# Kernel optimization log

Hardware: AMD Instinct MI355X
Metric: run time of the kernel (lower is better)

The kernel has to match this reference:

```python
import jax, jax.numpy as jnp
import numpy as np

E = 128  # embed_size


def setup_inputs() -> dict:
    key = jax.random.key(0)
    ks = jax.random.split(key, 20)
    NU, NI, NEV = 100000, 50000, 4096
    s = 0.05  # weight scale so softplus(dot) stays well-conditioned
    inp = {
        "user_emb": jax.random.normal(ks[0], (NU, E), jnp.float32) * s,
        "item_emb": jax.random.normal(ks[1], (NI, E), jnp.float32) * s,
        "ugru_wi": jax.random.normal(ks[2], (3 * E, E), jnp.float32) * s,
        "ugru_wh": jax.random.normal(ks[3], (3 * E, E), jnp.float32) * s,
        "ugru_bi": jax.random.normal(ks[4], (3 * E,), jnp.float32) * s,
        "ugru_bh": jax.random.normal(ks[5], (3 * E,), jnp.float32) * s,
        "igru_wi": jax.random.normal(ks[6], (3 * E, E), jnp.float32) * s,
        "igru_wh": jax.random.normal(ks[7], (3 * E, E), jnp.float32) * s,
        "igru_bi": jax.random.normal(ks[8], (3 * E,), jnp.float32) * s,
        "igru_bh": jax.random.normal(ks[9], (3 * E,), jnp.float32) * s,
        "t1_w": jax.random.normal(ks[10], (E, 2 * E), jnp.float32) * s,
        "t1_b": jax.random.normal(ks[11], (E,), jnp.float32) * s,
        "t2_w": jax.random.normal(ks[12], (32, E), jnp.float32) * s,
        "t2_b": jax.random.normal(ks[13], (32,), jnp.float32) * s,
        "t3_w": jax.random.normal(ks[14], (1, 32), jnp.float32) * s,
        "t3_b": jax.random.normal(ks[15], (1,), jnp.float32) * s,
        "user_ids": jax.random.randint(ks[16], (NEV,), 0, NU, jnp.int32),
        "item_ids": jax.random.randint(ks[17], (NEV,), 0, NI, jnp.int32),
    }
    return inp


def _gru(x, h, wi, wh, bi, bh):
    # torch.nn.GRUCell math, single sample: x,h [E]; wi,wh [3E,E]
    gi = wi @ x + bi
    gh = wh @ h + bh
    ir, iz, inn = jnp.split(gi, 3)
    hr, hz, hn = jnp.split(gh, 3)
    r = jax.nn.sigmoid(ir + hr)
    z = jax.nn.sigmoid(iz + hz)
    n = jnp.tanh(inn + r * hn)
    return (1.0 - z) * n + z * h


def reference(user_emb, item_emb, ugru_wi, ugru_wh, ugru_bi, ugru_bh,
              igru_wi, igru_wh, igru_bi, igru_bh,
              t1_w, t1_b, t2_w, t2_b, t3_w, t3_b,
              user_ids, item_ids):
    # Sequential event processing: per-event gather of user/item embedding,
    # Rayleigh base compatibility score, MLP (transForm1/2/3) branch score,
    # coupled GRUCell updates scattered back into the embedding tables.
    def step(carry, ev):
        U, V = carry
        u_id, i_id = ev
        u = U[u_id]          # [E] gather (dict-cache lookup in original)
        v = V[i_id]          # [E]
        comp = jax.nn.softplus(jnp.dot(u, v)) + 1e-10  # base_compatibility
        loss = -jnp.log(comp)                           # -log p(event)
        cat = jnp.concatenate([u, v])                   # [2E]
        h = jax.nn.relu(t1_w @ cat + t1_b)              # transForm1 + act
        h = jax.nn.relu(t2_w @ h + t2_b)                # transForm2 + act
        score = jax.nn.sigmoid(t3_w @ h + t3_b)[0]      # transForm3
        nu = _gru(v, u, ugru_wi, ugru_wh, ugru_bi, ugru_bh)  # user_cell
        nv = _gru(u, v, igru_wi, igru_wh, igru_bi, igru_bh)  # item_cell
        U = U.at[u_id].set(nu)  # coevolution scatter
        V = V.at[i_id].set(nv)
        return (U, V), jnp.stack([loss, score])

    (_, _), outs = jax.lax.scan(step, (user_emb, item_emb),
                                (user_ids, item_ids))
    return outs  # [num_events, 2] : (-log comp, branch score)
```

## Files before the change

kernel.cpp:

```cpp
#include <hip/hip_runtime.h>
#include <math.h>

#define EMB 128
#define MAXEV 4096
#define GEV 16

struct Hdr { int nl0; int nl1; int ncomp2; };

typedef __attribute__((ext_vector_type(8))) short bf16x8;
typedef __attribute__((ext_vector_type(4))) float f32x4;

__device__ __forceinline__ float sigmoidf_(float x) { return 1.0f / (1.0f + expf(-x)); }
__device__ __forceinline__ float softplusf_(float x) {
    return (x > 0.f) ? x + log1pf(expf(-x)) : log1pf(expf(x));
}
__device__ __forceinline__ unsigned short f2bf(float f) {
    unsigned int u = __float_as_uint(f);
    u += 0x7FFFu + ((u >> 16) & 1u);
    return (unsigned short)(u >> 16);
}
__device__ __forceinline__ float bf2f(unsigned short s) {
    return __uint_as_float((unsigned int)s << 16);
}

__global__ __launch_bounds__(64) void prev_kernel(
    const int* __restrict__ uids, const int* __restrict__ iids,
    int* __restrict__ prevu, int* __restrict__ previ, int nev,
    const float* __restrict__ Wuh, const float* __restrict__ Wii,
    const float* __restrict__ Wui, const float* __restrict__ Wih,
    const float* __restrict__ T1w, const float* __restrict__ T2w,
    unsigned short* __restrict__ wb_uh, unsigned short* __restrict__ wb_ii,
    unsigned short* __restrict__ wb_ui, unsigned short* __restrict__ wb_ih,
    unsigned short* __restrict__ t1wb, unsigned short* __restrict__ t2wb)
{
    int t = blockIdx.x;
    int lane = threadIdx.x;

    {
        int gid = t * 64 + lane;
        if (gid < 58368) {
            const float* src; unsigned short* dst; int q;
            if (gid < 49152) {
                int m = gid / 12288; q = gid - m * 12288;
                src = (m == 0) ? Wuh : (m == 1) ? Wii : (m == 2) ? Wui : Wih;
                dst = (m == 0) ? wb_uh : (m == 1) ? wb_ii : (m == 2) ? wb_ui : wb_ih;
            } else if (gid < 57344) { q = gid - 49152; src = T1w; dst = t1wb; }
            else                    { q = gid - 57344; src = T2w; dst = t2wb; }
            float4 v = ((const float4*)src)[q];
            *(ushort4*)(dst + (size_t)q * 4) =
                make_ushort4(f2bf(v.x), f2bf(v.y), f2bf(v.z), f2bf(v.w));
        }
    }

    if (t >= nev) return;
    int myu = uids[t], myi = iids[t];
    int bu = -1, bi = -1;
    for (int j = lane; j < t; j += 64) {
        if (uids[j] == myu) bu = j;
        if (iids[j] == myi) bi = j;
    }
    for (int off = 32; off; off >>= 1) {
        bu = max(bu, __shfl_xor(bu, off));
        bi = max(bi, __shfl_xor(bi, off));
    }
    if (lane == 0) { prevu[t] = bu; previ[t] = bi; }
}

__global__ __launch_bounds__(1024) void setup_kernel(
    const int* __restrict__ prevu, const int* __restrict__ previ,
    int* __restrict__ order0, int* __restrict__ order1,
    int* __restrict__ tail2Order, int* __restrict__ compStart,
    Hdr* __restrict__ hdr, int nev)
{
    __shared__ int   lab[MAXEV];
    __shared__ int   tmpT[MAXEV];
    __shared__ int   t2l[MAXEV];
    __shared__ short slev[MAXEV];
    __shared__ int   schanged, sn0, sn1, sn2, sntl;

    int tid = threadIdx.x;
    for (int t = tid; t < nev; t += 1024) slev[t] = 0;
    if (tid == 0) { sn0 = 0; sn1 = 0; sn2 = 0; sntl = 0; }
    __syncthreads();

    for (int t = tid; t < nev; t += 1024) {
        if (prevu[t] >= 0 || previ[t] >= 0) tmpT[atomicAdd(&sntl, 1)] = t;
        else                                 order0[atomicAdd(&sn0, 1)] = t;
    }
    __syncthreads();
    int ntl = sntl;

    for (int it = 0; it < nev; ++it) {
        if (tid == 0) schanged = 0;
        __syncthreads();
        for (int i = tid; i < ntl; i += 1024) {
            int t = tmpT[i];
            int pu = prevu[t], pi = previ[t];
            int nl = 0;
            if (pu >= 0) nl = slev[pu] + 1;
            if (pi >= 0) { int c = slev[pi] + 1; nl = nl > c ? nl : c; }
            if (nl > (int)slev[t]) { slev[t] = (short)nl; schanged = 1; }
        }
        __syncthreads();
        if (!schanged) break;
        __syncthreads();
    }

    for (int i = tid; i < ntl; i += 1024) {
        int t = tmpT[i];
        if (slev[t] == 1)      order1[atomicAdd(&sn1, 1)] = t;
        else if (slev[t] >= 2) t2l[atomicAdd(&sn2, 1)] = t;
    }
    __syncthreads();
    int n2 = sn2;

    for (int i = tid; i < n2; i += 1024) lab[t2l[i]] = t2l[i];
    __syncthreads();
    for (int it = 0; it < nev; ++it) {
        if (tid == 0) schanged = 0;
        __syncthreads();
        for (int i = tid; i < n2; i += 1024) {
            int t = t2l[i];
            int m = lab[t];
            int pu = prevu[t], pi = previ[t];
            bool eu = (pu >= 0 && slev[pu] >= 2);
            bool ei = (pi >= 0 && slev[pi] >= 2);
            if (eu) m = min(m, lab[pu]);
            if (ei) m = min(m, lab[pi]);
            if (m < lab[t]) { atomicMin(&lab[t], m); schanged = 1; }
            if (eu && m < lab[pu]) { atomicMin(&lab[pu], m); schanged = 1; }
            if (ei && m < lab[pi]) { atomicMin(&lab[pi], m); schanged = 1; }
        }
        __syncthreads();
        if (!schanged) break;
        __syncthreads();
    }

    for (int i = tid; i < n2; i += 1024) tmpT[i] = (lab[t2l[i]] << 12) | t2l[i];
    __syncthreads();
    for (int i = tid; i < n2; i += 1024) {
        int k = tmpT[i], r = 0;
        for (int j = 0; j < n2; ++j) r += (tmpT[j] < k);
        tail2Order[r] = k & 0xFFF;
    }
    __syncthreads();

    if (tid == 0) {
        int nc = 0;
        for (int i = 0; i < n2; ++i)
            if (i == 0 || lab[tail2Order[i]] != lab[tail2Order[i - 1]])
                compStart[nc++] = i;
        compStart[nc] = n2;
        hdr->ncomp2 = nc;
        hdr->nl0 = sn0;
        hdr->nl1 = sn1;
    }
}

__global__ __launch_bounds__(256) void gru_fused_kernel(
    const float* __restrict__ U0, const float* __restrict__ V0,
    const unsigned short* __restrict__ wb_ui, const unsigned short* __restrict__ wb_uh,
    const unsigned short* __restrict__ wb_ii, const unsigned short* __restrict__ wb_ih,
    const float* __restrict__ bui, const float* __restrict__ buh,
    const float* __restrict__ bii, const float* __restrict__ bih,
    const int* __restrict__ uids, const int* __restrict__ iids,
    const int* __restrict__ prevu, const int* __restrict__ previ,
    const float* NUr, const float* NVr,
    const int* __restrict__ order, const int* __restrict__ cnt_p,
    float* NU, float* NV)
{
    __shared__ __align__(16) unsigned short xbu[GEV][136];
    __shared__ __align__(16) unsigned short xbv[GEV][136];
    __shared__ float gg[GEV][772];

    int cnt = *cnt_p;
    int e0 = blockIdx.x * GEV;
    if (e0 >= cnt) return;

    int tid = threadIdx.x;
    int ev = tid >> 4, c8 = (tid & 15) * 8;

    {
        int e = e0 + ev;
        float4 a0, a1, c0, c1;
        if (e < cnt) {
            int t = order[e];
            int pu = prevu[t], pi = previ[t];
            const float* up = (pu < 0 ? U0 + (size_t)uids[t] * EMB : NUr + (size_t)pu * EMB) + c8;
            const float* vp = (pi < 0 ? V0 + (size_t)iids[t] * EMB : NVr + (size_t)pi * EMB) + c8;
            a0 = ((const float4*)up)[0]; a1 = ((const float4*)up)[1];
            c0 = ((const float4*)vp)[0]; c1 = ((const float4*)vp)[1];
        } else {
            a0 = make_float4(0.f, 0.f, 0.f, 0.f); a1 = a0; c0 = a0; c1 = a0;
        }
        *(ushort4*)&xbu[ev][c8]     = make_ushort4(f2bf(a0.x), f2bf(a0.y), f2bf(a0.z), f2bf(a0.w));
        *(ushort4*)&xbu[ev][c8 + 4] = make_ushort4(f2bf(a1.x), f2bf(a1.y), f2bf(a1.z), f2bf(a1.w));
        *(ushort4*)&xbv[ev][c8]     = make_ushort4(f2bf(c0.x), f2bf(c0.y), f2bf(c0.z), f2bf(c0.w));
        *(ushort4*)&xbv[ev][c8 + 4] = make_ushort4(f2bf(c1.x), f2bf(c1.y), f2bf(c1.z), f2bf(c1.w));
    }
    __syncthreads();

    int w = tid >> 6, l = tid & 63;
    int lr = l & 15, lk = (l >> 4) * 8;

    for (int ph = 0; ph < 2; ++ph) {
        const unsigned short* Wi = ph ? wb_ii : wb_ui;
        const unsigned short* Wh = ph ? wb_ih : wb_uh;
        const unsigned short (*Xi)[136] = ph ? xbu : xbv;
        const unsigned short (*Xh)[136] = ph ? xbv : xbu;

        f32x4 acc[12] = {};
        #pragma unroll
        for (int kk = 0; kk < 4; ++kk) {
            bf16x8 ai = *(const bf16x8*)&Xi[lr][kk * 32 + lk];
            bf16x8 ah = *(const bf16x8*)&Xh[lr][kk * 32 + lk];
            #pragma unroll
            for (int j = 0; j < 12; ++j) {
                int nt = w * 12 + j;
                bool ish = nt >= 24;
                int brow = (ish ? nt - 24 : nt) * 16 + lr;
                const unsigned short* W = ish ? Wh : Wi;
                bf16x8 b = *(const bf16x8*)(W + (size_t)brow * EMB + kk * 32 + lk);
                acc[j] = __builtin_amdgcn_mfma_f32_16x16x32_bf16(ish ? ah : ai, b, acc[j], 0, 0, 0);
            }
        }
        #pragma unroll
        for (int j = 0; j < 12; ++j) {
            int nt = w * 12 + j;
            #pragma unroll
            for (int i = 0; i < 4; ++i)
                gg[(l >> 4) * 4 + i][nt * 16 + lr] = acc[j][i];
        }
        __syncthreads();

        {
            int e = e0 + ev;
            if (e < cnt) {
                int t = order[e];
                const float* bi = ph ? bii : bui;
                const float* bh = ph ? bih : buh;
                float* N = ph ? NV : NU;
                const unsigned short (*xh)[136] = ph ? xbv : xbu;
                #pragma unroll
                for (int i = 0; i < 8; ++i) {
                    int ch = c8 + i;
                    float r_ = sigmoidf_(gg[ev][ch] + bi[ch] + gg[ev][384 + ch] + bh[ch]);
                    float z_ = sigmoidf_(gg[ev][128 + ch] + bi[128 + ch] + gg[ev][512 + ch] + bh[128 + ch]);
                    float n_ = tanhf(gg[ev][256 + ch] + bi[256 + ch] + r_ * (gg[ev][640 + ch] + bh[256 + ch]));
                    float h = bf2f(xh[ev][ch]);
                    N[(size_t)t * EMB + ch] = (1.f - z_) * n_ + z_ * h;
                }
            }
        }
        __syncthreads();
    }
}

__global__ __launch_bounds__(1024) void tail2_kernel(
    const float* __restrict__ U0,  const float* __restrict__ V0,
    const unsigned short* __restrict__ wb_ui, const unsigned short* __restrict__ wb_uh,
    const float* __restrict__ bui, const float* __restrict__ buh,
    const unsigned short* __restrict__ wb_ii, const unsigned short* __restrict__ wb_ih,
    const float* __restrict__ bii, const float* __restrict__ bih,
    const int* __restrict__ uids,  const int* __restrict__ iids,
    const int* __restrict__ prevu, const int* __restrict__ previ,
    const int* __restrict__ tail2Order, const int* __restrict__ compStart,
    const Hdr* __restrict__ hdr,
    float* __restrict__ NU, float* __restrict__ NV)
{
    __shared__ __align__(16) float su[EMB];
    __shared__ __align__(16) float sv[EMB];
    __shared__ float gg[1536];
    int tid = threadIdx.x;
    int ncomp = hdr->ncomp2;

    int g = tid >> 4, j = tid & 15;
    int mat = g >> 4;
    const unsigned short* W = (mat == 0) ? wb_ui : (mat == 1) ? wb_uh
                            : (mat == 2) ? wb_ii : wb_ih;

    for (int c = blockIdx.x; c < ncomp; c += gridDim.x) {
        int kb = compStart[c], ke = compStart[c + 1];
        for (int k = kb; k < ke; ++k) {
            int t = tail2Order[k];
            int pu = prevu[t], pi = previ[t];
            const float* up = (pu < 0) ? U0 + (size_t)uids[t] * EMB : NU + (size_t)pu * EMB;
            const float* vp = (pi < 0) ? V0 + (size_t)iids[t] * EMB : NV + (size_t)pi * EMB;
            __syncthreads();
            if (tid < EMB)        su[tid] = up[tid];
            else if (tid < 2*EMB) sv[tid - EMB] = vp[tid - EMB];
            __syncthreads();

            const float* x = (mat == 1 || mat == 2) ? su : sv;
            float x8[8];
            #pragma unroll
            for (int i = 0; i < 8; ++i) x8[i] = x[j * 8 + i];

            #pragma unroll 1
            for (int b = 0; b < 2; ++b) {
                int rbase = (g & 15) * 24 + b * 12;
                bf16x8 wv[12];
                #pragma unroll
                for (int q = 0; q < 12; ++q)
                    wv[q] = *(const bf16x8*)(W + (size_t)(rbase + q) * EMB + j * 8);
                #pragma unroll
                for (int q = 0; q < 12; ++q) {
                    float s = bf2f((unsigned short)wv[q][0]) * x8[0]
                            + bf2f((unsigned short)wv[q][1]) * x8[1]
                            + bf2f((unsigned short)wv[q][2]) * x8[2]
                            + bf2f((unsigned short)wv[q][3]) * x8[3]
                            + bf2f((unsigned short)wv[q][4]) * x8[4]
                            + bf2f((unsigned short)wv[q][5]) * x8[5]
                            + bf2f((unsigned short)wv[q][6]) * x8[6]
                            + bf2f((unsigned short)wv[q][7]) * x8[7];
                    s += __shfl_xor(s, 1); s += __shfl_xor(s, 2);
                    s += __shfl_xor(s, 4); s += __shfl_xor(s, 8);
                    if (j == (q & 15)) gg[mat * 384 + rbase + q] = s;
                }
            }
            __syncthreads();

            if (tid < EMB) {
                int e = tid;
                float r_ = sigmoidf_(gg[e] + bui[e] + gg[384 + e] + buh[e]);
                float z_ = sigmoidf_(gg[128 + e] + bui[128 + e] + gg[512 + e] + buh[128 + e]);
                float n_ = tanhf(gg[256 + e] + bui[256 + e] + r_ * (gg[640 + e] + buh[256 + e]));
                NU[(size_t)t * EMB + e] = (1.f - z_) * n_ + z_ * su[e];
            } else if (tid < 2*EMB) {
                int e = tid - EMB;
                float r_ = sigmoidf_(gg[768 + e] + bii[e] + gg[1152 + e] + bih[e]);
                float z_ = sigmoidf_(gg[896 + e] + bii[128 + e] + gg[1280 + e] + bih[128 + e]);
                float n_ = tanhf(gg[1024 + e] + bii[256 + e] + r_ * (gg[1408 + e] + bih[256 + e]));
                NV[(size_t)t * EMB + e] = (1.f - z_) * n_ + z_ * sv[e];
            }
        }
    }
}

__global__ __launch_bounds__(256) void post_fused_kernel(
    const float* __restrict__ U0, const float* __restrict__ V0,
    const int* __restrict__ uids, const int* __restrict__ iids,
    const int* __restrict__ prevu, const int* __restrict__ previ,
    const float* __restrict__ NU, const float* __restrict__ NV,
    const unsigned short* __restrict__ t1wb, const float* __restrict__ T1b,
    const unsigned short* __restrict__ t2wb, const float* __restrict__ T2b,
    const float* __restrict__ T3w, const float* __restrict__ T3b,
    float* __restrict__ out, int nev)
{
    __shared__ __align__(16) unsigned short xau[64][136];
    __shared__ __align__(16) unsigned short xav[64][136];
    __shared__ __align__(16) unsigned short h1b[64][136];
    __shared__ float h2s[64][36];

    int tid = threadIdx.x;
    int ev0 = blockIdx.x * 64;

    #pragma unroll
    for (int rep = 0; rep < 4; ++rep) {
        int idx = rep * 256 + tid;
        int evl = idx >> 4, j16 = idx & 15;
        int t = ev0 + evl;
        float4 a0, a1, c0, c1;
        if (t < nev) {
            int pu = prevu[t], pi = previ[t];
            const float* up = (pu < 0 ? U0 + (size_t)uids[t] * EMB : NU + (size_t)pu * EMB) + j16 * 8;
            const float* vp = (pi < 0 ? V0 + (size_t)iids[t] * EMB : NV + (size_t)pi * EMB) + j16 * 8;
            a0 = ((const float4*)up)[0]; a1 = ((const float4*)up)[1];
            c0 = ((const float4*)vp)[0]; c1 = ((const float4*)vp)[1];
        } else {
            a0 = make_float4(0.f, 0.f, 0.f, 0.f); a1 = a0; c0 = a0; c1 = a0;
        }
        *(ushort4*)&xau[evl][j16 * 8]     = make_ushort4(f2bf(a0.x), f2bf(a0.y), f2bf(a0.z), f2bf(a0.w));
        *(ushort4*)&xau[evl][j16 * 8 + 4] = make_ushort4(f2bf(a1.x), f2bf(a1.y), f2bf(a1.z), f2bf(a1.w));
        *(ushort4*)&xav[evl][j16 * 8]     = make_ushort4(f2bf(c0.x), f2bf(c0.y), f2bf(c0.z), f2bf(c0.w));
        *(ushort4*)&xav[evl][j16 * 8 + 4] = make_ushort4(f2bf(c1.x), f2bf(c1.y), f2bf(c1.z), f2bf(c1.w));
        float dp = a0.x * c0.x + a0.y * c0.y + a0.z * c0.z + a0.w * c0.w
                 + a1.x * c1.x + a1.y * c1.y + a1.z * c1.z + a1.w * c1.w;
        dp += __shfl_xor(dp, 1); dp += __shfl_xor(dp, 2);
        dp += __shfl_xor(dp, 4); dp += __shfl_xor(dp, 8);
        if (j16 == 0 && t < nev)
            out[2 * (size_t)t] = -logf(softplusf_(dp) + 1e-10f);
    }
    __syncthreads();

    int w = tid >> 6, l = tid & 63;
    int lr = l & 15, lk = (l >> 4) * 8;

    {
        f32x4 acc[8] = {};
        #pragma unroll
        for (int kh = 0; kh < 8; ++kh) {
            const unsigned short* ar = (kh < 4)
                ? &xau[w * 16 + lr][kh * 32 + lk]
                : &xav[w * 16 + lr][(kh - 4) * 32 + lk];
            bf16x8 a = *(const bf16x8*)ar;
            #pragma unroll
            for (int n = 0; n < 8; ++n) {
                bf16x8 b = *(const bf16x8*)(t1wb + (size_t)(n * 16 + lr) * 256 + kh * 32 + lk);
                acc[n] = __builtin_amdgcn_mfma_f32_16x16x32_bf16(a, b, acc[n], 0, 0, 0);
            }
        }
        #pragma unroll
        for (int n = 0; n < 8; ++n) {
            int col = n * 16 + lr;
            float bb = T1b[col];
            #pragma unroll
            for (int i = 0; i < 4; ++i)
                h1b[w * 16 + (l >> 4) * 4 + i][col] = f2bf(fmaxf(acc[n][i] + bb, 0.f));
        }
    }
    __syncthreads();

    {
        f32x4 acc2[2] = {};
        #pragma unroll
        for (int kk = 0; kk < 4; ++kk) {
            bf16x8 a = *(const bf16x8*)&h1b[w * 16 + lr][kk * 32 + lk];
            #pragma unroll
            for (int n = 0; n < 2; ++n) {
                bf16x8 b = *(const bf16x8*)(t2wb + (size_t)(n * 16 + lr) * 128 + kk * 32 + lk);
                acc2[n] = __builtin_amdgcn_mfma_f32_16x16x32_bf16(a, b, acc2[n], 0, 0, 0);
            }
        }
        #pragma unroll
        for (int n = 0; n < 2; ++n) {
            int col = n * 16 + lr;
            float bb = T2b[col];
            #pragma unroll
            for (int i = 0; i < 4; ++i)
                h2s[w * 16 + (l >> 4) * 4 + i][col] = fmaxf(acc2[n][i] + bb, 0.f);
        }
    }
    __syncthreads();

    {
        int evl = tid >> 2, q4 = tid & 3;
        float p = 0.f;
        #pragma unroll
        for (int i = 0; i < 8; ++i) {
            int ch = q4 * 8 + i;
            p = fmaf(T3w[ch], h2s[evl][ch], p);
        }
        p += __shfl_xor(p, 1); p += __shfl_xor(p, 2);
        int t = ev0 + evl;
        if (q4 == 0 && t < nev)
            out[2 * (size_t)t + 1] = sigmoidf_(p + T3b[0]);
    }
}

extern "C" void kernel_launch(void* const* d_in, const int* in_sizes, int n_in,
                              void* d_out, int out_size, void* d_ws, size_t ws_size,
                              hipStream_t stream)
{
    const float* U0  = (const float*)d_in[0];
    const float* V0  = (const float*)d_in[1];
    const float* Wui = (const float*)d_in[2];
    const float* Wuh = (const float*)d_in[3];
    const float* bui = (const float*)d_in[4];
    const float* buh = (const float*)d_in[5];
    const float* Wii = (const float*)d_in[6];
    const float* Wih = (const float*)d_in[7];
    const float* bii = (const float*)d_in[8];
    const float* bih = (const float*)d_in[9];
    const float* T1w = (const float*)d_in[10];
    const float* T1b = (const float*)d_in[11];
    const float* T2w = (const float*)d_in[12];
    const float* T2b = (const float*)d_in[13];
    const float* T3w = (const float*)d_in[14];
    const float* T3b = (const float*)d_in[15];
    const int* uids  = (const int*)d_in[16];
    const int* iids  = (const int*)d_in[17];
    int nev = in_sizes[16];

    char* ws = (char*)d_ws;
    int* base = (int*)ws;
    int* prevu      = base;
    int* previ      = base + MAXEV;
    int* order0     = base + 2 * MAXEV;
    int* order1     = base + 3 * MAXEV;
    int* tail2Order = base + 4 * MAXEV;
    int* compStart  = base + 5 * MAXEV;
    Hdr* hdr        = (Hdr*)(base + 6 * MAXEV + 4);
    float* NU = (float*)(ws + (160 << 10));
    float* NV = NU + (size_t)MAXEV * EMB;
    unsigned short* wb_uh = (unsigned short*)(NV + (size_t)MAXEV * EMB);
    unsigned short* wb_ii = wb_uh + 384 * EMB;
    unsigned short* wb_ui = wb_ii + 384 * EMB;
    unsigned short* wb_ih = wb_ui + 384 * EMB;
    unsigned short* t1wb  = wb_ih + 384 * EMB;
    unsigned short* t2wb  = t1wb + EMB * 256;
    float* out = (float*)d_out;

    prev_kernel<<<MAXEV, 64, 0, stream>>>(
        uids, iids, prevu, previ, nev,
        Wuh, Wii, Wui, Wih, T1w, T2w,
        wb_uh, wb_ii, wb_ui, wb_ih, t1wb, t2wb);
    setup_kernel<<<1, 1024, 0, stream>>>(prevu, previ, order0, order1,
                                         tail2Order, compStart, hdr, nev);

    gru_fused_kernel<<<MAXEV / GEV, 256, 0, stream>>>(
        U0, V0, wb_ui, wb_uh, wb_ii, wb_ih, bui, buh, bii, bih,
        uids, iids, prevu, previ, NU, NV, order0, &hdr->nl0, NU, NV);

    gru_fused_kernel<<<MAXEV / GEV, 256, 0, stream>>>(
        U0, V0, wb_ui, wb_uh, wb_ii, wb_ih, bui, buh, bii, bih,
        uids, iids, prevu, previ, NU, NV, order1, &hdr->nl1, NU, NV);

    tail2_kernel<<<64, 1024, 0, stream>>>(
        U0, V0, wb_ui, wb_uh, bui, buh, wb_ii, wb_ih, bii, bih,
        uids, iids, prevu, previ, tail2Order, compStart, hdr, NU, NV);

    post_fused_kernel<<<(nev + 63) / 64, 256, 0, stream>>>(
        U0, V0, uids, iids, prevu, previ, NU, NV,
        t1wb, T1b, t2wb, T2b, T3w, T3b, out, nev);
}
```

Before: 105.5 us.

## Fuse loss and MLP score computation into GRU and tail kernels

```diff
diff --git a/kernel.cpp b/kernel.cpp
--- a/kernel.cpp
+++ b/kernel.cpp
@@ -163,15 +163,20 @@
     const unsigned short* __restrict__ wb_ii, const unsigned short* __restrict__ wb_ih,
     const float* __restrict__ bui, const float* __restrict__ buh,
     const float* __restrict__ bii, const float* __restrict__ bih,
+    const unsigned short* __restrict__ t1wb, const float* __restrict__ T1b,
+    const unsigned short* __restrict__ t2wb, const float* __restrict__ T2b,
+    const float* __restrict__ T3w, const float* __restrict__ T3b,
     const int* __restrict__ uids, const int* __restrict__ iids,
     const int* __restrict__ prevu, const int* __restrict__ previ,
     const float* NUr, const float* NVr,
     const int* __restrict__ order, const int* __restrict__ cnt_p,
-    float* NU, float* NV)
+    float* NU, float* NV, float* __restrict__ out)
 {
     __shared__ __align__(16) unsigned short xbu[GEV][136];
     __shared__ __align__(16) unsigned short xbv[GEV][136];
-    __shared__ float gg[GEV][772];
+    __shared__ __align__(16) float gg[GEV][772];
+    unsigned short (*h1b)[136] = (unsigned short (*)[136])&gg[0][0];
+    float (*h2s)[36] = (float (*)[36])&gg[2][0];
 
     int cnt = *cnt_p;
     int e0 = blockIdx.x * GEV;
@@ -182,9 +187,10 @@
 
     {
         int e = e0 + ev;
+        int t = -1;
         float4 a0, a1, c0, c1;
         if (e < cnt) {
-            int t = order[e];
+            t = order[e];
             int pu = prevu[t], pi = previ[t];
             const float* up = (pu < 0 ? U0 + (size_t)uids[t] * EMB : NUr + (size_t)pu * EMB) + c8;
             const float* vp = (pi < 0 ? V0 + (size_t)iids[t] * EMB : NVr + (size_t)pi * EMB) + c8;
@@ -197,6 +203,12 @@
         *(ushort4*)&xbu[ev][c8 + 4] = make_ushort4(f2bf(a1.x), f2bf(a1.y), f2bf(a1.z), f2bf(a1.w));
         *(ushort4*)&xbv[ev][c8]     = make_ushort4(f2bf(c0.x), f2bf(c0.y), f2bf(c0.z), f2bf(c0.w));
         *(ushort4*)&xbv[ev][c8 + 4] = make_ushort4(f2bf(c1.x), f2bf(c1.y), f2bf(c1.z), f2bf(c1.w));
+        float dp = a0.x * c0.x + a0.y * c0.y + a0.z * c0.z + a0.w * c0.w
+                 + a1.x * c1.x + a1.y * c1.y + a1.z * c1.z + a1.w * c1.w;
+        dp += __shfl_xor(dp, 1); dp += __shfl_xor(dp, 2);
+        dp += __shfl_xor(dp, 4); dp += __shfl_xor(dp, 8);
+        if ((tid & 15) == 0 && t >= 0)
+            out[2 * (size_t)t] = -logf(softplusf_(dp) + 1e-10f);
     }
     __syncthreads();
 
@@ -254,6 +266,60 @@
         }
         __syncthreads();
     }
+
+    {
+        f32x4 acc1[2] = {};
+        #pragma unroll
+        for (int kh = 0; kh < 8; ++kh) {
+            bf16x8 a = (kh < 4) ? *(const bf16x8*)&xbu[lr][kh * 32 + lk]
+                                : *(const bf16x8*)&xbv[lr][(kh - 4) * 32 + lk];
+            #pragma unroll
+            for (int n = 0; n < 2; ++n) {
+                int nt = w * 2 + n;
+                bf16x8 b = *(const bf16x8*)(t1wb + (size_t)(nt * 16 + lr) * 256 + kh * 32 + lk);
+                acc1[n] = __builtin_amdgcn_mfma_f32_16x16x32_bf16(a, b, acc1[n], 0, 0, 0);
+            }
+        }
+        #pragma unroll
+        for (int n = 0; n < 2; ++n) {
+            int col = (w * 2 + n) * 16 + lr;
+            float bb = T1b[col];
+            #pragma unroll
+            for (int i = 0; i < 4; ++i)
+                h1b[(l >> 4) * 4 + i][col] = f2bf(fmaxf(acc1[n][i] + bb, 0.f));
+        }
+    }
+    __syncthreads();
+
+    if (w < 2) {
+        f32x4 acc2 = {};
+        #pragma unroll
+        for (int kk = 0; kk < 4; ++kk) {
+            bf16x8 a = *(const bf16x8*)&h1b[lr][kk * 32 + lk];
+            bf16x8 b = *(const bf16x8*)(t2wb + (size_t)(w * 16 + lr) * 128 + kk * 32 + lk);
+            acc2 = __builtin_amdgcn_mfma_f32_16x16x32_bf16(a, b, acc2, 0, 0, 0);
+        }
+        int col = w * 16 + lr;
+        float bb = T2b[col];
+        #pragma unroll
+        for (int i = 0; i < 4; ++i)
+            h2s[(l >> 4) * 4 + i][col] = fmaxf(acc2[i] + bb, 0.f);
+    }
+    __syncthreads();
+
+    if (tid < 64) {
+        int evl = tid >> 2, q4 = tid & 3;
+        float p = 0.f;
+        #pragma unroll
+        for (int i = 0; i < 8; ++i) {
+            int ch = q4 * 8 + i;
+            p = fmaf(T3w[ch], h2s[evl][ch], p);
+        }
+        p += __shfl_xor(p, 1); p += __shfl_xor(p, 2);
+        int e = e0 + evl;
+        if (q4 == 0 && e < cnt)
+            out[2 * (size_t)order[e] + 1] = sigmoidf_(p + T3b[0]);
+    }
 }
 
 __global__ __launch_bounds__(1024) void tail2_kernel(
@@ -262,11 +328,14 @@
     const float* __restrict__ bui, const float* __restrict__ buh,
     const unsigned short* __restrict__ wb_ii, const unsigned short* __restrict__ wb_ih,
     const float* __restrict__ bii, const float* __restrict__ bih,
+    const float* __restrict__ T1w, const float* __restrict__ T1b,
+    const float* __restrict__ T2w, const float* __restrict__ T2b,
+    const float* __restrict__ T3w, const float* __restrict__ T3b,
     const int* __restrict__ uids,  const int* __restrict__ iids,
     const int* __restrict__ prevu, const int* __restrict__ previ,
     const int* __restrict__ tail2Order, const int* __restrict__ compStart,
     const Hdr* __restrict__ hdr,
-    float* __restrict__ NU, float* __restrict__ NV)
+    float* __restrict__ NU, float* __restrict__ NV, float* __restrict__ out)
 {
     __shared__ __align__(16) float su[EMB];
     __shared__ __align__(16) float sv[EMB];
@@ -333,118 +402,46 @@
                 float n_ = tanhf(gg[1024 + e] + bii[256 + e] + r_ * (gg[1408 + e] + bih[256 + e]));
                 NV[(size_t)t * EMB + e] = (1.f - z_) * n_ + z_ * sv[e];
             }
-        }
-    }
-}
-
-__global__ __launch_bounds__(256) void post_fused_kernel(
-    const float* __restrict__ U0, const float* __restrict__ V0,
-    const int* __restrict__ uids, const int* __restrict__ iids,
-    const int* __restrict__ prevu, const int* __restrict__ previ,
-    const float* __restrict__ NU, const float* __restrict__ NV,
-    const unsigned short* __restrict__ t1wb, const float* __restrict__ T1b,
-    const unsigned short* __restrict__ t2wb, const float* __restrict__ T2b,
-    const float* __restrict__ T3w, const float* __restrict__ T3b,
-    float* __restrict__ out, int nev)
-{
-    __shared__ __align__(16) unsigned short xau[64][136];
-    __shared__ __align__(16) unsigned short xav[64][136];
-    __shared__ __align__(16) unsigned short h1b[64][136];
-    __shared__ float h2s[64][36];
-
-    int tid = threadIdx.x;
-    int ev0 = blockIdx.x * 64;
-
-    #pragma unroll
-    for (int rep = 0; rep < 4; ++rep) {
-        int idx = rep * 256 + tid;
-        int evl = idx >> 4, j16 = idx & 15;
-        int t = ev0 + evl;
-        float4 a0, a1, c0, c1;
-        if (t < nev) {
-            int pu = prevu[t], pi = previ[t];
-            const float* up = (pu < 0 ? U0 + (size_t)uids[t] * EMB : NU + (size_t)pu * EMB) + j16 * 8;
-            const float* vp = (pi < 0 ? V0 + (size_t)iids[t] * EMB : NV + (size_t)pi * EMB) + j16 * 8;
-            a0 = ((const float4*)up)[0]; a1 = ((const float4*)up)[1];
-            c0 = ((const float4*)vp)[0]; c1 = ((const float4*)vp)[1];
-        } else {
-            a0 = make_float4(0.f, 0.f, 0.f, 0.f); a1 = a0; c0 = a0; c1 = a0;
-        }
-        *(ushort4*)&xau[evl][j16 * 8]     = make_ushort4(f2bf(a0.x), f2bf(a0.y), f2bf(a0.z), f2bf(a0.w));
-        *(ushort4*)&xau[evl][j16 * 8 + 4] = make_ushort4(f2bf(a1.x), f2bf(a1.y), f2bf(a1.z), f2bf(a1.w));
-        *(ushort4*)&xav[evl][j16 * 8]     = make_ushort4(f2bf(c0.x), f2bf(c0.y), f2bf(c0.z), f2bf(c0.w));
-        *(ushort4*)&xav[evl][j16 * 8 + 4] = make_ushort4(f2bf(c1.x), f2bf(c1.y), f2bf(c1.z), f2bf(c1.w));
-        float dp = a0.x * c0.x + a0.y * c0.y + a0.z * c0.z + a0.w * c0.w
-                 + a1.x * c1.x + a1.y * c1.y + a1.z * c1.z + a1.w * c1.w;
-        dp += __shfl_xor(dp, 1); dp += __shfl_xor(dp, 2);
-        dp += __shfl_xor(dp, 4); dp += __shfl_xor(dp, 8);
-        if (j16 == 0 && t < nev)
-            out[2 * (size_t)t] = -logf(softplusf_(dp) + 1e-10f);
-    }
-    __syncthreads();
-
-    int w = tid >> 6, l = tid & 63;
-    int lr = l & 15, lk = (l >> 4) * 8;
-
-    {
-        f32x4 acc[8] = {};
-        #pragma unroll
-        for (int kh = 0; kh < 8; ++kh) {
-            const unsigned short* ar = (kh < 4)
-                ? &xau[w * 16 + lr][kh * 32 + lk]
-                : &xav[w * 16 + lr][(kh - 4) * 32 + lk];
-            bf16x8 a = *(const bf16x8*)ar;
-            #pragma unroll
-            for (int n = 0; n < 8; ++n) {
-                bf16x8 b = *(const bf16x8*)(t1wb + (size_t)(n * 16 + lr) * 256 + kh * 32 + lk);
-                acc[n] = __builtin_amdgcn_mfma_f32_16x16x32_bf16(a, b, acc[n], 0, 0, 0);
-            }
-        }
-        #pragma unroll
-        for (int n = 0; n < 8; ++n) {
-            int col = n * 16 + lr;
-            float bb = T1b[col];
-            #pragma unroll
-            for (int i = 0; i < 4; ++i)
-                h1b[w * 16 + (l >> 4) * 4 + i][col] = f2bf(fmaxf(acc[n][i] + bb, 0.f));
-        }
-    }
-    __syncthreads();
-
-    {
-        f32x4 acc2[2] = {};
-        #pragma unroll
-        for (int kk = 0; kk < 4; ++kk) {
-            bf16x8 a = *(const bf16x8*)&h1b[w * 16 + lr][kk * 32 + lk];
-            #pragma unroll
-            for (int n = 0; n < 2; ++n) {
-                bf16x8 b = *(const bf16x8*)(t2wb + (size_t)(n * 16 + lr) * 128 + kk * 32 + lk);
-                acc2[n] = __builtin_amdgcn_mfma_f32_16x16x32_bf16(a, b, acc2[n], 0, 0, 0);
-            }
-        }
-        #pragma unroll
-        for (int n = 0; n < 2; ++n) {
-            int col = n * 16 + lr;
-            float bb = T2b[col];
-            #pragma unroll
-            for (int i = 0; i < 4; ++i)
-                h2s[w * 16 + (l >> 4) * 4 + i][col] = fmaxf(acc2[n][i] + bb, 0.f);
-        }
-    }
-    __syncthreads();
-
-    {
-        int evl = tid >> 2, q4 = tid & 3;
-        float p = 0.f;
-        #pragma unroll
-        for (int i = 0; i < 8; ++i) {
-            int ch = q4 * 8 + i;
-            p = fmaf(T3w[ch], h2s[evl][ch], p);
-        }
-        p += __shfl_xor(p, 1); p += __shfl_xor(p, 2);
-        int t = ev0 + evl;
-        if (q4 == 0 && t < nev)
-            out[2 * (size_t)t + 1] = sigmoidf_(p + T3b[0]);
+            __syncthreads();
+
+            if (tid < 64) {
+                float p = su[tid] * sv[tid] + su[tid + 64] * sv[tid + 64];
+                p += __shfl_xor(p, 1);  p += __shfl_xor(p, 2);
+                p += __shfl_xor(p, 4);  p += __shfl_xor(p, 8);
+                p += __shfl_xor(p, 16); p += __shfl_xor(p, 32);
+                if (tid == 0) out[2 * (size_t)t] = -logf(softplusf_(p) + 1e-10f);
+            }
+            {
+                int r = tid >> 3, kq = tid & 7;
+                float s = 0.f;
+                #pragma unroll
+                for (int kk = 0; kk < 32; ++kk) {
+                    int kx = kq * 32 + kk;
+                    s = fmaf(T1w[(size_t)r * 256 + kx],
+                             (kx < 128) ? su[kx] : sv[kx - 128], s);
+                }
+                s += __shfl_xor(s, 1); s += __shfl_xor(s, 2); s += __shfl_xor(s, 4);
+                if (kq == 0) gg[r] = fmaxf(s + T1b[r], 0.f);
+            }
+            __syncthreads();
+            {
+                int r2 = tid >> 5, kq = tid & 31;
+                float s = 0.f;
+                #pragma unroll
+                for (int kk = 0; kk < 4; ++kk)
+                    s = fmaf(T2w[(size_t)r2 * 128 + kq * 4 + kk], gg[kq * 4 + kk], s);
+                s += __shfl_xor(s, 1); s += __shfl_xor(s, 2);
+                s += __shfl_xor(s, 4); s += __shfl_xor(s, 8); s += __shfl_xor(s, 16);
+                if (kq == 0) gg[200 + r2] = fmaxf(s + T2b[r2], 0.f);
+            }
+            __syncthreads();
+            if (tid < 32) {
+                float p = T3w[tid] * gg[200 + tid];
+                p += __shfl_xor(p, 1); p += __shfl_xor(p, 2);
+                p += __shfl_xor(p, 4); p += __shfl_xor(p, 8); p += __shfl_xor(p, 16);
+                if (tid == 0) out[2 * (size_t)t + 1] = sigmoidf_(p + T3b[0]);
+            }
+        }
     }
 }
 
@@ -500,17 +497,16 @@
 
     gru_fused_kernel<<<MAXEV / GEV, 256, 0, stream>>>(
         U0, V0, wb_ui, wb_uh, wb_ii, wb_ih, bui, buh, bii, bih,
-        uids, iids, prevu, previ, NU, NV, order0, &hdr->nl0, NU, NV);
+        t1wb, T1b, t2wb, T2b, T3w, T3b,
+        uids, iids, prevu, previ, NU, NV, order0, &hdr->nl0, NU, NV, out);
 
     gru_fused_kernel<<<MAXEV / GEV, 256, 0, stream>>>(
         U0, V0, wb_ui, wb_uh, wb_ii, wb_ih, bui, buh, bii, bih,
-        uids, iids, prevu, previ, NU, NV, order1, &hdr->nl1, NU, NV);
+        t1wb, T1b, t2wb, T2b, T3w, T3b,
+        uids, iids, prevu, previ, NU, NV, order1, &hdr->nl1, NU, NV, out);
 
     tail2_kernel<<<64, 1024, 0, stream>>>(
         U0, V0, wb_ui, wb_uh, bui, buh, wb_ii, wb_ih, bii, bih,
-        uids, iids, prevu, previ, tail2Order, compStart, hdr, NU, NV);
-
-    post_fused_kernel<<<(nev + 63) / 64, 256, 0, stream>>>(
-        U0, V0, uids, iids, prevu, previ, NU, NV,
-        t1wb, T1b, t2wb, T2b, T3w, T3b, out, nev);
-}
+        T1w, T1b, T2w, T2b, T3w, T3b,
+        uids, iids, prevu, previ, tail2Order, compStart, hdr, NU, NV, out);
+}
```

Result: no change. 105.2 us (-0.3%).
